# Optimization experiments

Hardware: AMD Instinct MI355X
Metric: run time of the kernel (lower is better)

Reference implementation:

```python
import jax, jax.numpy as jnp
import numpy as np

E = 800_000   # number of scattered elements (edges)
Q = 50_000    # number of queries (segments)
D = 128       # in_embed_dim == in_queries_dim == qk_proj_dim


def setup_inputs() -> dict:
    key = jax.random.key(0)
    k_sv, k_idx, k_q, k_wq, k_bq, k_wk, k_bk = jax.random.split(key, 7)
    lim = 1.0 / np.sqrt(D)
    return {
        "scattered_values": jax.random.normal(k_sv, (E, D), dtype=jnp.float32),
        "indices": jax.random.randint(k_idx, (E,), 0, Q, dtype=jnp.int32),
        "queries": jax.random.normal(k_q, (Q, D), dtype=jnp.float32),
        "Wq": jax.random.uniform(k_wq, (D, D), jnp.float32, -lim, lim),
        "bq": jax.random.uniform(k_bq, (D,), jnp.float32, -lim, lim),
        "Wk": jax.random.uniform(k_wk, (D, D), jnp.float32, -lim, lim),
        "bk": jax.random.uniform(k_bk, (D,), jnp.float32, -lim, lim),
    }


def reference(scattered_values, indices, queries, Wq, bq, Wk, bk):
    num_segments = queries.shape[0]
    proj_dim = Wq.shape[1]

    # Project queries [Q, P] then gather per element -> [E, P]
    q_proj = queries @ Wq + bq
    q_gathered = q_proj[indices]

    # Project keys [E, P]
    keys = scattered_values @ Wk + bk

    # Per-element dot-product scores, scaled
    scale = proj_dim ** (-0.5)
    probs = jnp.einsum("ed,ed->e", keys, q_gathered) * scale  # [E]

    # Segment (scatter) softmax over elements sharing the same index
    seg_max = jax.ops.segment_max(probs, indices, num_segments=num_segments)
    ex = jnp.exp(probs - seg_max[indices])
    seg_sum = jax.ops.segment_sum(ex, indices, num_segments=num_segments)
    scores = ex / seg_sum[indices]  # [E]

    # Weighted scatter-sum of (unprojected) values -> [Q, D]
    attn_applied = jax.ops.segment_sum(
        scattered_values * scores[:, None], indices, num_segments=num_segments
    )
    return scores, attn_applied
```

## Files before the change

### kernel.cpp

```cpp
#include <hip/hip_runtime.h>
#include <math.h>

#define DD 128

__global__ void k_zero(int* p, int n) {
    int i = blockIdx.x * blockDim.x + threadIdx.x;
    if (i < n) p[i] = 0;
}

__global__ void k_precompute(const float* __restrict__ Wq, const float* __restrict__ bq,
                             const float* __restrict__ Wk, const float* __restrict__ bk,
                             float* __restrict__ M, float* __restrict__ tvec,
                             float* __restrict__ uvec, float* __restrict__ s0) {
    __shared__ float wkT[64][129];
    __shared__ float wqrow[128];
    __shared__ float bqs[128];
    const int dp  = blockIdx.x;
    const int tid = threadIdx.x;
    wqrow[tid] = Wq[dp * DD + tid];
    bqs[tid]   = bq[tid];
    float acc = 0.f, tacc = 0.f;
    for (int ch = 0; ch < 2; ++ch) {
        __syncthreads();
        for (int i = tid; i < 128 * 64; i += 128) {
            int d = i >> 6, j = i & 63;
            wkT[j][d] = Wk[d * DD + ch * 64 + j];
        }
        __syncthreads();
        #pragma unroll 8
        for (int j = 0; j < 64; ++j) {
            float w = wkT[j][tid];
            acc  += wqrow[ch * 64 + j] * w;
            tacc += bqs[ch * 64 + j] * w;
        }
    }
    M[dp * DD + tid] = acc;
    if (dp == 0) {
        tvec[tid] = tacc;
        float ua = 0.f;
        for (int p = 0; p < DD; ++p) ua += Wq[tid * DD + p] * bk[p];
        uvec[tid] = ua;
        if (tid == 0) {
            float s = 0.f;
            for (int p = 0; p < DD; ++p) s += bq[p] * bk[p];
            *s0 = s;
        }
    }
}

__global__ __launch_bounds__(256) void k_gemm(const float* __restrict__ queries,
                                              const float* __restrict__ M,
                                              const float* __restrict__ tvec,
                                              float* __restrict__ zs, int Q, float scale) {
    __shared__ __align__(16) float Ms[32 * 128];
    __shared__ float qs[64 * 33];
    const int t  = threadIdx.x;
    const int tx = t & 15;
    const int ty = t >> 4;
    const int qbase = blockIdx.x * 64;
    float acc[4][8];
    #pragma unroll
    for (int j = 0; j < 4; ++j)
        #pragma unroll
        for (int i = 0; i < 8; ++i) acc[j][i] = 0.f;

    for (int kc = 0; kc < 4; ++kc) {
        __syncthreads();
        for (int i = t; i < 1024; i += 256) {
            int r = i >> 5, c4 = i & 31;
            ((float4*)Ms)[r * 32 + c4] = ((const float4*)(M + (size_t)(kc * 32 + r) * DD))[c4];
        }
        for (int i = t; i < 2048; i += 256) {
            int r = i >> 5, c = i & 31;
            int q = qbase + r;
            qs[r * 33 + c] = (q < Q) ? queries[(size_t)q * DD + kc * 32 + c] : 0.f;
        }
        __syncthreads();
        #pragma unroll 8
        for (int k = 0; k < 32; ++k) {
            float4 ma = *(const float4*)&Ms[k * 128 + tx * 8];
            float4 mb = *(const float4*)&Ms[k * 128 + tx * 8 + 4];
            float mv[8] = {ma.x, ma.y, ma.z, ma.w, mb.x, mb.y, mb.z, mb.w};
            #pragma unroll
            for (int j = 0; j < 4; ++j) {
                float qv = qs[(ty * 4 + j) * 33 + k];
                #pragma unroll
                for (int i = 0; i < 8; ++i) acc[j][i] = fmaf(qv, mv[i], acc[j][i]);
            }
        }
    }
    float4 t0 = *(const float4*)(tvec + tx * 8);
    float4 t1 = *(const float4*)(tvec + tx * 8 + 4);
    float tv[8] = {t0.x, t0.y, t0.z, t0.w, t1.x, t1.y, t1.z, t1.w};
    #pragma unroll
    for (int j = 0; j < 4; ++j) {
        int q = qbase + ty * 4 + j;
        if (q < Q) {
            float o[8];
            #pragma unroll
            for (int i = 0; i < 8; ++i) o[i] = (acc[j][i] + tv[i]) * scale;
            float4 w0 = {o[0], o[1], o[2], o[3]};
            float4 w1 = {o[4], o[5], o[6], o[7]};
            *(float4*)(zs + (size_t)q * DD + tx * 8)     = w0;
            *(float4*)(zs + (size_t)q * DD + tx * 8 + 4) = w1;
        }
    }
}

__global__ void k_hist(const int* __restrict__ idx, int* __restrict__ hist, int E) {
    int i = blockIdx.x * blockDim.x + threadIdx.x;
    if (i < E) atomicAdd(&hist[idx[i]], 1);
}

__global__ void k_scan1(const int* __restrict__ hist, int* __restrict__ bsum, int Q) {
    int i = blockIdx.x * 256 + threadIdx.x;
    int v = (i < Q) ? hist[i] : 0;
    #pragma unroll
    for (int off = 1; off < 64; off <<= 1) v += __shfl_xor(v, off);
    __shared__ int sd[4];
    if ((threadIdx.x & 63) == 0) sd[threadIdx.x >> 6] = v;
    __syncthreads();
    if (threadIdx.x == 0) bsum[blockIdx.x] = sd[0] + sd[1] + sd[2] + sd[3];
}

__global__ void k_scan2(const int* __restrict__ bsum, int* __restrict__ boff, int NB) {
    __shared__ int s[256];
    int t = threadIdx.x;
    int v = (t < NB) ? bsum[t] : 0;
    s[t] = v;
    __syncthreads();
    for (int off = 1; off < 256; off <<= 1) {
        int add = (t >= off) ? s[t - off] : 0;
        __syncthreads();
        s[t] += add;
        __syncthreads();
    }
    if (t < NB) boff[t] = s[t] - v;
}

__global__ void k_scan3(const int* __restrict__ hist, const int* __restrict__ boff,
                        int* __restrict__ seg_start, int* __restrict__ cursor, int Q) {
    __shared__ int s[256];
    int t = threadIdx.x;
    int i = blockIdx.x * 256 + t;
    int v = (i < Q) ? hist[i] : 0;
    s[t] = v;
    __syncthreads();
    for (int off = 1; off < 256; off <<= 1) {
        int add = (t >= off) ? s[t - off] : 0;
        __syncthreads();
        s[t] += add;
        __syncthreads();
    }
    if (i < Q) {
        int excl = s[t] - v + boff[blockIdx.x];
        seg_start[i] = excl;
        cursor[i]    = excl;
    }
}

__global__ void k_scatter(const int* __restrict__ idx, int* __restrict__ cursor,
                          int* __restrict__ perm, int E) {
    int i = blockIdx.x * blockDim.x + threadIdx.x;
    if (i < E) {
        int q   = idx[i];
        int pos = atomicAdd(&cursor[q], 1);
        perm[pos] = i;
    }
}

#define EXCAP 512
__global__ __launch_bounds__(256) void k_attn(const float* __restrict__ SV,
                                              const float* __restrict__ queries,
                                              const float* __restrict__ uvec,
                                              const float* __restrict__ s0ptr,
                                              const int* __restrict__ hist,
                                              const int* __restrict__ seg_start,
                                              const int* __restrict__ perm,
                                              float* __restrict__ zs_attn,
                                              float* __restrict__ scores,
                                              int Q, float scale) {
    __shared__ float exbuf[4][EXCAP];
    const int wid  = threadIdx.x >> 6;
    const int lane = threadIdx.x & 63;
    const int q    = blockIdx.x * 4 + wid;
    const bool act = (q < Q);

    float2 zv = make_float2(0.f, 0.f), qv2 = zv, uv2 = zv;
    int cnt = 0, start = 0;
    if (act) {
        zv    = ((const float2*)(zs_attn + (size_t)q * DD))[lane];
        qv2   = ((const float2*)(queries + (size_t)q * DD))[lane];
        uv2   = ((const float2*)uvec)[lane];
        cnt   = hist[q];
        start = seg_start[q];
    }
    float cd = qv2.x * uv2.x + qv2.y * uv2.y;
    #pragma unroll
    for (int off = 1; off < 64; off <<= 1) cd += __shfl_xor(cd, off);
    float cq = (cd + s0ptr[0]) * scale;

    float accx = 0.f, accy = 0.f, ssum = 0.f;
    for (int base = 0; base < cnt; base += 64) {
        int m  = min(64, cnt - base);
        int pe = (lane < m) ? perm[start + base + lane] : 0;
        int e0 = __shfl(pe, 0);
        float2 sv = ((const float2*)(SV + (size_t)e0 * DD))[lane];
        for (int i = 0; i < m; ++i) {
            float2 svn = make_float2(0.f, 0.f);
            if (i + 1 < m) {
                int en = __shfl(pe, i + 1);
                svn = ((const float2*)(SV + (size_t)en * DD))[lane];
            }
            float p = fmaf(sv.x, zv.x, sv.y * zv.y);
            #pragma unroll
            for (int off = 1; off < 64; off <<= 1) p += __shfl_xor(p, off);
            float ex = __expf(p + cq);
            ssum += ex;
            accx = fmaf(ex, sv.x, accx);
            accy = fmaf(ex, sv.y, accy);
            if (lane == 0 && (base + i) < EXCAP) exbuf[wid][base + i] = ex;
            sv = svn;
        }
    }
    __syncthreads();
    if (act) {
        float2* arow = (float2*)(zs_attn + (size_t)q * DD);
        if (cnt == 0) {
            arow[lane] = make_float2(0.f, 0.f);
        } else {
            float inv = 1.f / ssum;
            arow[lane] = make_float2(accx * inv, accy * inv);
            int lim = min(cnt, EXCAP);
            for (int i = lane; i < lim; i += 64)
                scores[perm[start + i]] = exbuf[wid][i] * inv;
        }
    }
}

extern "C" void kernel_launch(void* const* d_in, const int* in_sizes, int n_in,
                              void* d_out, int out_size, void* d_ws, size_t ws_size,
                              hipStream_t stream) {
    const float* SV      = (const float*)d_in[0];
    const int*   indices = (const int*)d_in[1];
    const float* queries = (const float*)d_in[2];
    const float* Wq      = (const float*)d_in[3];
    const float* bq      = (const float*)d_in[4];
    const float* Wk      = (const float*)d_in[5];
    const float* bk      = (const float*)d_in[6];

    const int E = in_sizes[1];
    const int Q = in_sizes[2] / DD;
    const float scale = 1.0f / sqrtf((float)DD);

    float* scores  = (float*)d_out;
    float* zs_attn = (float*)d_out + E;

    float* ws   = (float*)d_ws;
    float* M    = ws;
    float* tvec = ws + 16384;
    float* uvec = ws + 16512;
    float* s0   = ws + 16640;
    int* hist      = (int*)ws + 16896;
    int* seg_start = hist + Q;
    int* cursor    = seg_start + Q;
    int* bsum      = cursor + Q;
    int* boff      = bsum + 256;
    int* perm      = boff + 256;

    const int NB = (Q + 255) / 256;

    hipLaunchKernelGGL(k_zero, dim3(NB), dim3(256), 0, stream, hist, Q);
    hipLaunchKernelGGL(k_precompute, dim3(128), dim3(128), 0, stream,
                       Wq, bq, Wk, bk, M, tvec, uvec, s0);
    hipLaunchKernelGGL(k_gemm, dim3((Q + 63) / 64), dim3(256), 0, stream,
                       queries, M, tvec, zs_attn, Q, scale);
    hipLaunchKernelGGL(k_hist, dim3((E + 255) / 256), dim3(256), 0, stream,
                       indices, hist, E);
    hipLaunchKernelGGL(k_scan1, dim3(NB), dim3(256), 0, stream, hist, bsum, Q);
    hipLaunchKernelGGL(k_scan2, dim3(1), dim3(256), 0, stream, bsum, boff, NB);
    hipLaunchKernelGGL(k_scan3, dim3(NB), dim3(256), 0, stream,
                       hist, boff, seg_start, cursor, Q);
    hipLaunchKernelGGL(k_scatter, dim3((E + 255) / 256), dim3(256), 0, stream,
                       indices, cursor, perm, E);
    hipLaunchKernelGGL(k_attn, dim3((Q + 3) / 4), dim3(256), 0, stream,
                       SV, queries, uvec, s0, hist, seg_start, perm,
                       zs_attn, scores, Q, scale);
}
```

Before: 750.5 us.

## Fuse init and scan kernels, unroll attention loop by four, add rescale pass

Merges the hist zeroing into the weight precompute kernel, and merges scan1 and scan2 into one kernel that uses a last-block ticket to run the offset scan. The attention loop now handles four edges per iteration with independent shuffle reductions, giving more memory-level parallelism than the one-ahead prefetch. Unnormalised scores are written directly and a new elementwise kernel rescales them by a per-segment inverse sum, which drops the shared buffer and its size cap. This adds a full extra pass over scores and indices, plus scattered single-lane stores inside the loop.

Measured after the change: 737.1 us. About the same (-1.8%).

```diff
diff --git a/kernel.cpp b/kernel.cpp
--- a/kernel.cpp
+++ b/kernel.cpp
@@ -3,20 +3,24 @@
 
 #define DD 128
 
-__global__ void k_zero(int* p, int n) {
-    int i = blockIdx.x * blockDim.x + threadIdx.x;
-    if (i < n) p[i] = 0;
-}
-
-__global__ void k_precompute(const float* __restrict__ Wq, const float* __restrict__ bq,
-                             const float* __restrict__ Wk, const float* __restrict__ bk,
-                             float* __restrict__ M, float* __restrict__ tvec,
-                             float* __restrict__ uvec, float* __restrict__ s0) {
+__global__ void k_init(const float* __restrict__ Wq, const float* __restrict__ bq,
+                       const float* __restrict__ Wk, const float* __restrict__ bk,
+                       float* __restrict__ M, float* __restrict__ tvec,
+                       float* __restrict__ uvec, float* __restrict__ s0,
+                       int* __restrict__ hist, int* __restrict__ done,
+                       int Q, int NB) {
+    const int tid = threadIdx.x;
+    if (blockIdx.x < (unsigned)NB) {
+        int base = blockIdx.x * 256;
+        for (int j = base + tid; j < base + 256; j += 128)
+            if (j < Q) hist[j] = 0;
+        if (blockIdx.x == 0 && tid == 0) *done = 0;
+        return;
+    }
     __shared__ float wkT[64][129];
     __shared__ float wqrow[128];
     __shared__ float bqs[128];
-    const int dp  = blockIdx.x;
-    const int tid = threadIdx.x;
+    const int dp = blockIdx.x - NB;
     wqrow[tid] = Wq[dp * DD + tid];
     bqs[tid]   = bq[tid];
     float acc = 0.f, tacc = 0.f;
@@ -112,30 +116,38 @@
     if (i < E) atomicAdd(&hist[idx[i]], 1);
 }
 
-__global__ void k_scan1(const int* __restrict__ hist, int* __restrict__ bsum, int Q) {
-    int i = blockIdx.x * 256 + threadIdx.x;
+__global__ void k_scan12(const int* __restrict__ hist, int* __restrict__ bsum,
+                         int* __restrict__ boff, int* __restrict__ done,
+                         int Q, int NB) {
+    const int t = threadIdx.x;
+    int i = blockIdx.x * 256 + t;
     int v = (i < Q) ? hist[i] : 0;
     #pragma unroll
     for (int off = 1; off < 64; off <<= 1) v += __shfl_xor(v, off);
     __shared__ int sd[4];
-    if ((threadIdx.x & 63) == 0) sd[threadIdx.x >> 6] = v;
+    __shared__ int ticket;
+    if ((t & 63) == 0) sd[t >> 6] = v;
     __syncthreads();
-    if (threadIdx.x == 0) bsum[blockIdx.x] = sd[0] + sd[1] + sd[2] + sd[3];
-}
-
-__global__ void k_scan2(const int* __restrict__ bsum, int* __restrict__ boff, int NB) {
-    __shared__ int s[256];
-    int t = threadIdx.x;
-    int v = (t < NB) ? bsum[t] : 0;
-    s[t] = v;
+    if (t == 0) {
+        bsum[blockIdx.x] = sd[0] + sd[1] + sd[2] + sd[3];
+        __threadfence();
+        ticket = atomicAdd(done, 1);
+    }
     __syncthreads();
-    for (int off = 1; off < 256; off <<= 1) {
-        int add = (t >= off) ? s[t - off] : 0;
-        __syncthreads();
-        s[t] += add;
-        __syncthreads();
-    }
-    if (t < NB) boff[t] = s[t] - v;
+    if (ticket == NB - 1) {
+        __threadfence();
+        __shared__ int s[256];
+        int vv = (t < NB) ? bsum[t] : 0;
+        s[t] = vv;
+        __syncthreads();
+        for (int off = 1; off < 256; off <<= 1) {
+            int add = (t >= off) ? s[t - off] : 0;
+            __syncthreads();
+            s[t] += add;
+            __syncthreads();
+        }
+        if (t < NB) boff[t] = s[t] - vv;
+    }
 }
 
 __global__ void k_scan3(const int* __restrict__ hist, const int* __restrict__ boff,
@@ -169,7 +181,6 @@
     }
 }
 
-#define EXCAP 512
 __global__ __launch_bounds__(256) void k_attn(const float* __restrict__ SV,
                                               const float* __restrict__ queries,
                                               const float* __restrict__ uvec,
@@ -179,63 +190,81 @@
                                               const int* __restrict__ perm,
                                               float* __restrict__ zs_attn,
                                               float* __restrict__ scores,
+                                              float* __restrict__ invsum,
                                               int Q, float scale) {
-    __shared__ float exbuf[4][EXCAP];
     const int wid  = threadIdx.x >> 6;
     const int lane = threadIdx.x & 63;
     const int q    = blockIdx.x * 4 + wid;
-    const bool act = (q < Q);
-
-    float2 zv = make_float2(0.f, 0.f), qv2 = zv, uv2 = zv;
-    int cnt = 0, start = 0;
-    if (act) {
-        zv    = ((const float2*)(zs_attn + (size_t)q * DD))[lane];
-        qv2   = ((const float2*)(queries + (size_t)q * DD))[lane];
-        uv2   = ((const float2*)uvec)[lane];
-        cnt   = hist[q];
-        start = seg_start[q];
-    }
-    float cd = qv2.x * uv2.x + qv2.y * uv2.y;
+    if (q >= Q) return;
+
+    float2 zv  = ((const float2*)(zs_attn + (size_t)q * DD))[lane];
+    float2 qv2 = ((const float2*)(queries + (size_t)q * DD))[lane];
+    float2 uv2 = ((const float2*)uvec)[lane];
+    float cd = fmaf(qv2.x, uv2.x, qv2.y * uv2.y);
     #pragma unroll
     for (int off = 1; off < 64; off <<= 1) cd += __shfl_xor(cd, off);
-    float cq = (cd + s0ptr[0]) * scale;
+    const float cq = (cd + s0ptr[0]) * scale;
+
+    const int cnt   = hist[q];
+    const int start = seg_start[q];
 
     float accx = 0.f, accy = 0.f, ssum = 0.f;
     for (int base = 0; base < cnt; base += 64) {
-        int m  = min(64, cnt - base);
-        int pe = (lane < m) ? perm[start + base + lane] : 0;
-        int e0 = __shfl(pe, 0);
-        float2 sv = ((const float2*)(SV + (size_t)e0 * DD))[lane];
-        for (int i = 0; i < m; ++i) {
-            float2 svn = make_float2(0.f, 0.f);
-            if (i + 1 < m) {
-                int en = __shfl(pe, i + 1);
-                svn = ((const float2*)(SV + (size_t)en * DD))[lane];
+        const int m = min(64, cnt - base);
+        int pe = perm[start + base + ((lane < m) ? lane : 0)];
+        for (int i = 0; i < m; i += 4) {
+            const int i1 = min(i + 1, m - 1);
+            const int i2 = min(i + 2, m - 1);
+            const int i3 = min(i + 3, m - 1);
+            const int e0 = __shfl(pe, i);
+            const int e1 = __shfl(pe, i1);
+            const int e2 = __shfl(pe, i2);
+            const int e3 = __shfl(pe, i3);
+            const float2 s0v = ((const float2*)(SV + (size_t)e0 * DD))[lane];
+            const float2 s1v = ((const float2*)(SV + (size_t)e1 * DD))[lane];
+            const float2 s2v = ((const float2*)(SV + (size_t)e2 * DD))[lane];
+            const float2 s3v = ((const float2*)(SV + (size_t)e3 * DD))[lane];
+            float p0 = fmaf(s0v.x, zv.x, s0v.y * zv.y);
+            float p1 = fmaf(s1v.x, zv.x, s1v.y * zv.y);
+            float p2 = fmaf(s2v.x, zv.x, s2v.y * zv.y);
+            float p3 = fmaf(s3v.x, zv.x, s3v.y * zv.y);
+            #pragma unroll
+            for (int off = 1; off < 64; off <<= 1) {
+                p0 += __shfl_xor(p0, off);
+                p1 += __shfl_xor(p1, off);
+                p2 += __shfl_xor(p2, off);
+                p3 += __shfl_xor(p3, off);
             }
-            float p = fmaf(sv.x, zv.x, sv.y * zv.y);
-            #pragma unroll
-            for (int off = 1; off < 64; off <<= 1) p += __shfl_xor(p, off);
-            float ex = __expf(p + cq);
-            ssum += ex;
-            accx = fmaf(ex, sv.x, accx);
-            accy = fmaf(ex, sv.y, accy);
-            if (lane == 0 && (base + i) < EXCAP) exbuf[wid][base + i] = ex;
-            sv = svn;
-        }
-    }
-    __syncthreads();
-    if (act) {
-        float2* arow = (float2*)(zs_attn + (size_t)q * DD);
-        if (cnt == 0) {
-            arow[lane] = make_float2(0.f, 0.f);
-        } else {
-            float inv = 1.f / ssum;
-            arow[lane] = make_float2(accx * inv, accy * inv);
-            int lim = min(cnt, EXCAP);
-            for (int i = lane; i < lim; i += 64)
-                scores[perm[start + i]] = exbuf[wid][i] * inv;
-        }
-    }
+            const float ex0 = __expf(p0 + cq);
+            const float ex1 = (i + 1 < m) ? __expf(p1 + cq) : 0.f;
+            const float ex2 = (i + 2 < m) ? __expf(p2 + cq) : 0.f;
+            const float ex3 = (i + 3 < m) ? __expf(p3 + cq) : 0.f;
+            ssum += (ex0 + ex1) + (ex2 + ex3);
+            accx = fmaf(ex0, s0v.x, fmaf(ex1, s1v.x, fmaf(ex2, s2v.x, fmaf(ex3, s3v.x, accx))));
+            accy = fmaf(ex0, s0v.y, fmaf(ex1, s1v.y, fmaf(ex2, s2v.y, fmaf(ex3, s3v.y, accy))));
+            if (lane == 0) {
+                scores[e0] = ex0;
+                if (i + 1 < m) scores[e1] = ex1;
+                if (i + 2 < m) scores[e2] = ex2;
+                if (i + 3 < m) scores[e3] = ex3;
+            }
+        }
+    }
+
+    float2* arow = (float2*)(zs_attn + (size_t)q * DD);
+    if (cnt == 0) {
+        arow[lane] = make_float2(0.f, 0.f);
+    } else {
+        const float inv = 1.f / ssum;
+        arow[lane] = make_float2(accx * inv, accy * inv);
+        if (lane == 0) invsum[q] = inv;
+    }
+}
+
+__global__ void k_rescale(const int* __restrict__ idx, const float* __restrict__ invsum,
+                          float* __restrict__ scores, int E) {
+    int i = blockIdx.x * blockDim.x + threadIdx.x;
+    if (i < E) scores[i] = scores[i] * invsum[idx[i]];
 }
 
 extern "C" void kernel_launch(void* const* d_in, const int* in_sizes, int n_in,
@@ -261,29 +290,32 @@
     float* tvec = ws + 16384;
     float* uvec = ws + 16512;
     float* s0   = ws + 16640;
-    int* hist      = (int*)ws + 16896;
+    int* hist      = (int*)ws + 17024;
     int* seg_start = hist + Q;
     int* cursor    = seg_start + Q;
     int* bsum      = cursor + Q;
     int* boff      = bsum + 256;
-    int* perm      = boff + 256;
+    int* done      = boff + 256;
+    int* perm      = done + 64;
+    float* invsum  = (float*)(perm + E);
 
     const int NB = (Q + 255) / 256;
 
-    hipLaunchKernelGGL(k_zero, dim3(NB), dim3(256), 0, stream, hist, Q);
-    hipLaunchKernelGGL(k_precompute, dim3(128), dim3(128), 0, stream,
-                       Wq, bq, Wk, bk, M, tvec, uvec, s0);
+    hipLaunchKernelGGL(k_init, dim3(NB + 128), dim3(128), 0, stream,
+                       Wq, bq, Wk, bk, M, tvec, uvec, s0, hist, done, Q, NB);
     hipLaunchKernelGGL(k_gemm, dim3((Q + 63) / 64), dim3(256), 0, stream,
                        queries, M, tvec, zs_attn, Q, scale);
     hipLaunchKernelGGL(k_hist, dim3((E + 255) / 256), dim3(256), 0, stream,
                        indices, hist, E);
-    hipLaunchKernelGGL(k_scan1, dim3(NB), dim3(256), 0, stream, hist, bsum, Q);
-    hipLaunchKernelGGL(k_scan2, dim3(1), dim3(256), 0, stream, bsum, boff, NB);
+    hipLaunchKernelGGL(k_scan12, dim3(NB), dim3(256), 0, stream,
+                       hist, bsum, boff, done, Q, NB);
     hipLaunchKernelGGL(k_scan3, dim3(NB), dim3(256), 0, stream,
                        hist, boff, seg_start, cursor, Q);
     hipLaunchKernelGGL(k_scatter, dim3((E + 255) / 256), dim3(256), 0, stream,
                        indices, cursor, perm, E);
     hipLaunchKernelGGL(k_attn, dim3((Q + 3) / 4), dim3(256), 0, stream,
                        SV, queries, uvec, s0, hist, seg_start, perm,
-                       zs_attn, scores, Q, scale);
-}
+                       zs_attn, scores, invsum, Q, scale);
+    hipLaunchKernelGGL(k_rescale, dim3((E + 255) / 256), dim3(256), 0, stream,
+                       indices, invsum, scores, E);
+}
```
